# Performance work log

Hardware: AMD Instinct MI355X
Metric: run time of the kernel (lower is better)

## Reference

```python
import jax, jax.numpy as jnp
import numpy as np
from jax import lax

KERNEL = 2
STACKS = 2
LAYERS = 10
DILATIONS = [2 ** l for _ in range(STACKS) for l in range(LAYERS)]  # 20 blocks
RECEPTIVE_FIELD = sum((KERNEL - 1) * d for d in DILATIONS)  # 2046


def setup_inputs() -> dict:
    key = jax.random.key(0)
    ks = jax.random.split(key, 8)
    B, L, C, NC = 8, 4096, 256, 256
    NB = len(DILATIONS)
    SK = L - RECEPTIVE_FIELD  # 2050

    def rn(k, shape, scale):
        return jax.random.normal(k, shape, jnp.float32) * scale

    return {
        "input_x": jax.random.normal(ks[0], (B, L, 1), jnp.float32),
        "causal_w": rn(ks[1], (1, C), 1.0),                 # 1x1 causal conv, in=1
        "causal_b": jnp.zeros((C,), jnp.float32),
        "dil_w": rn(ks[2], (NB, KERNEL, C, C), (KERNEL * C) ** -0.5),  # WIO per block
        "dil_b": jnp.zeros((NB, C), jnp.float32),
        "res_w": rn(ks[3], (NB, C, C), C ** -0.5),
        "res_b": jnp.zeros((NB, C), jnp.float32),
        "skip_w": rn(ks[4], (NB, C, C), C ** -0.5),
        "skip_b": jnp.zeros((NB, C), jnp.float32),
        "cls_conv_w": rn(ks[5], (C, C), C ** -0.5),
        "cls_conv_b": jnp.zeros((C,), jnp.float32),
        "dense_w": rn(ks[6], (SK * C, NC), (SK * C) ** -0.5),
        "dense_b": jnp.zeros((NC,), jnp.float32),
    }


def _conv1x1(x, w, b):
    # x: [B, T, Cin], w: [Cin, Cout]
    return jnp.einsum("btc,co->bto", x, w) + b


def _dilated_causal_conv(x, w, b, d):
    # keras 'causal' pad followed by slicing off the first (k-1)*d frames
    # is exactly a VALID dilated conv. x: [B,T,Cin], w: [K,Cin,Cout]
    y = lax.conv_general_dilated(
        x, w, window_strides=(1,), padding="VALID", rhs_dilation=(d,),
        dimension_numbers=("NWC", "WIO", "NWC"))
    return y + b


def reference(input_x, causal_w, causal_b, dil_w, dil_b, res_w, res_b,
              skip_w, skip_b, cls_conv_w, cls_conv_b, dense_w, dense_b):
    # initial causal conv (kernel_size=1 -> plain 1x1 conv)
    x = _conv1x1(input_x, causal_w, causal_b)  # [B, L, C]
    skip_size = x.shape[1] - RECEPTIVE_FIELD

    skips = []
    for i, d in enumerate(DILATIONS):
        h = _dilated_causal_conv(x, dil_w[i], dil_b[i], d)  # [B, T-(k-1)d, C]
        g = jnp.tanh(h) * jax.nn.sigmoid(h)                  # gated activation
        res = _conv1x1(g, res_w[i], res_b[i])
        x = res + g                                          # residual (same length)
        s = _conv1x1(g, skip_w[i], skip_b[i])[:, -skip_size:]
        skips.append(s)

    # classifier head: mean over blocks, relu, shared 1x1 conv twice, dense+softmax
    s = jnp.mean(jnp.stack(skips, 0), axis=0)  # [B, skip_size, C]
    s = jax.nn.relu(s)
    s = _conv1x1(s, cls_conv_w, cls_conv_b)
    s = jax.nn.relu(s)
    s = _conv1x1(s, cls_conv_w, cls_conv_b)    # same conv applied twice (shared weights)
    f = s.reshape(s.shape[0], -1)              # flatten [B, skip_size*C]
    logits = f @ dense_w + dense_b
    return jax.nn.softmax(logits, axis=-1)
```

## Files before the change

### kernel.cpp

```cpp
#include <hip/hip_runtime.h>

typedef __attribute__((ext_vector_type(8))) short short8;
typedef __attribute__((ext_vector_type(4))) float f32x4;
typedef unsigned int uint32;
typedef unsigned short u16;

#define CCH   256
#define BATCH 8
#define LFULL 4096
#define SKL   2050
#define BM    64
#define BN    128
#define LDKC  72

#define GSTRIDE ((size_t)BATCH * LFULL * CCH)
#define XSTR    ((size_t)LFULL * CCH)
#define SSTR    ((size_t)SKL * CCH)
#define PSTR    ((size_t)BATCH * SKL * CCH)

__device__ const int TOUT[20] = {4095,4093,4089,4081,4065,4033,3969,3841,3585,3073,
                                 3072,3070,3066,3058,3042,3010,2946,2818,2562,2050};

__device__ __forceinline__ u16 f2b(float f) {
  uint32 u = __float_as_uint(f);
  u += 0x7fff + ((u >> 16) & 1);
  return (u16)(u >> 16);
}
__device__ __forceinline__ float gatef(float h) {
  float hc = fmaxf(h, -30.0f);
  float q = __expf(-hc);
  return (1.0f - q) * __builtin_amdgcn_rcpf(fmaf(q, q, 1.0f));
}
__device__ __forceinline__ void glds16(const void* g, void* l) {
  __builtin_amdgcn_global_load_lds(
      (const __attribute__((address_space(1))) void*)g,
      (__attribute__((address_space(3))) void*)l, 16, 0, 0);
}
__device__ __forceinline__ int xcd_swz(int orig, int nwg) {
  int xcd = orig & 7, idx = orig >> 3;
  int q = nwg >> 3, r = nwg & 7;
  int base = (xcd < r) ? xcd * (q + 1) : r * (q + 1) + (xcd - r) * q;
  return base + idx;
}

__global__ __launch_bounds__(256)
void prep_all(const float* __restrict__ res_w, const float* __restrict__ dil_w,
              const float* __restrict__ dil_b, const float* __restrict__ res_b,
              const float* __restrict__ causal_w, const float* __restrict__ causal_b,
              const float* __restrict__ skip_w, const float* __restrict__ cls_w,
              const float* __restrict__ skip_b,
              u16* __restrict__ DWP, float* __restrict__ Bc, float* __restrict__ U,
              u16* __restrict__ SWP, u16* __restrict__ CW, float* __restrict__ SBS) {
  __shared__ float As[32][256];
  const int bx = blockIdx.x;
  const int tid = threadIdx.x;

  if (bx < 304) {
    int chunk = bx & 7, tap = (bx >> 3) & 1, bi = bx >> 4;
    int i = bi + 1;
    int co = tid;
    int ci0 = chunk * 32;

    for (int idx = tid; idx < 32 * 256; idx += 256) {
      int r = idx >> 8, m = idx & 255;
      float v = res_w[((size_t)(bi * 256 + ci0 + r)) * 256 + m];
      if (ci0 + r == m) v += 1.0f;
      As[r][m] = v;
    }
    __syncthreads();

    float acc[32];
    #pragma unroll
    for (int r = 0; r < 32; ++r) acc[r] = 0.0f;

    const float* Wb = dil_w + ((size_t)(i * 2 + tap) * 256) * 256 + co;
    for (int m4 = 0; m4 < 64; ++m4) {
      const float* wp = Wb + (size_t)m4 * 4 * 256;
      float w0 = wp[0], w1 = wp[256], w2 = wp[512], w3 = wp[768];
      #pragma unroll
      for (int r = 0; r < 32; ++r) {
        float4 a = *(const float4*)&As[r][m4 * 4];
        acc[r] = fmaf(a.x, w0, acc[r]);
        acc[r] = fmaf(a.y, w1, acc[r]);
        acc[r] = fmaf(a.z, w2, acc[r]);
        acc[r] = fmaf(a.w, w3, acc[r]);
      }
    }
    int kb = tap * 8 + chunk;
    int kt = kb >> 1, ks = kb & 1;
    int ny = co >> 7, wn = (co >> 6) & 1, fn = (co >> 4) & 3, fr = co & 15;
    u16* ob = DWP + (size_t)bi * 131072 + kt * 16384 + ks * 8192 +
              ny * 4096 + wn * 2048 + fn * 512 + fr * 8;
    #pragma unroll
    for (int g = 0; g < 4; ++g) {
      u16 tmp[8];
      #pragma unroll
      for (int jj = 0; jj < 8; ++jj) tmp[jj] = f2b(acc[g * 8 + jj]);
      *(uint4*)(ob + g * 128) = *(uint4*)tmp;
    }
  } else if (bx < 304 + 5120) {
    int e = (bx - 304) * 256 + tid;
    int co = e & 255, ci = (e >> 8) & 255, i = e >> 16;
    int kk = ci >> 6, ks = (ci >> 5) & 1, fq = (ci >> 3) & 3, jj = ci & 7;
    int ny = co >> 7, wn = (co >> 6) & 1, fn = (co >> 4) & 3, fr = co & 15;
    int lane = fq * 16 + fr;
    SWP[(size_t)i * 65536 + kk * 16384 + ks * 8192 + ny * 4096 + wn * 2048 +
        fn * 512 + lane * 8 + jj] = f2b(skip_w[e]);
  } else if (bx < 304 + 5120 + 256) {
    int e = (bx - 5424) * 256 + tid;
    int co = e & 255, ci = e >> 8;
    CW[(size_t)co * 256 + ci] = f2b(cls_w[e]);
  } else if (bx < 5680 + 19) {
    int bi = bx - 5680, i = bi + 1, co = tid;
    float acc = dil_b[(size_t)i * 256 + co];
    const float* W0 = dil_w + ((size_t)(i * 2 + 0) * 256) * 256;
    const float* W1 = dil_w + ((size_t)(i * 2 + 1) * 256) * 256;
    for (int m = 0; m < 256; ++m) {
      float rb = res_b[(size_t)bi * 256 + m];
      acc = fmaf(rb, W0[(size_t)m * 256 + co] + W1[(size_t)m * 256 + co], acc);
    }
    Bc[(size_t)bi * 256 + co] = acc;
  } else if (bx == 5699) {
    int co = tid;
    float u0 = 0.f, u1 = 0.f, b0 = dil_b[co];
    for (int m = 0; m < 256; ++m) {
      float cwm = causal_w[m], cbm = causal_b[m];
      float w0 = dil_w[(size_t)m * 256 + co];
      float w1 = dil_w[(size_t)(256 + m) * 256 + co];
      u0 = fmaf(cwm, w0, u0);
      u1 = fmaf(cwm, w1, u1);
      b0 = fmaf(cbm, w0 + w1, b0);
    }
    U[co] = u0; U[256 + co] = u1; U[512 + co] = b0;
  } else {
    int n = tid;
    float s = 0.f;
    for (int i = 0; i < 20; ++i) s += skip_b[(size_t)i * 256 + n];
    SBS[n] = s;
  }
}

__global__ __launch_bounds__(256)
void g0_init(const float* __restrict__ in, const float* __restrict__ U,
             u16* __restrict__ G0) {
  int t = blockIdx.x, b = blockIdx.y, co = threadIdx.x;
  float x0 = in[(size_t)b * LFULL + t];
  float x1 = in[(size_t)b * LFULL + t + 1];
  float h = fmaf(x0, U[co], fmaf(x1, U[256 + co], U[512 + co]));
  G0[((size_t)b * LFULL + t) * CCH + co] = f2b(gatef(h));
}

__global__ __launch_bounds__(256)
void gatem(const u16* __restrict__ Ain, int d, int Tout, int ntile,
           const u16* __restrict__ Wp, const float* __restrict__ bias,
           u16* __restrict__ Gout) {
  __shared__ u16 As[3][BM * 64];

  const int tid = threadIdx.x;
  const int nwg = ntile * 16;
  const int wgid = xcd_swz(blockIdx.x, nwg);
  const int tx = wgid % ntile;
  const int rem = wgid / ntile;
  const int ny = rem & 1;
  const int bb = rem >> 1;

  const int t0 = tx * BM;
  const int n0 = ny * BN;
  const int lane = tid & 63, wv = tid >> 6;
  const int wm = wv >> 1, wn = wv & 1;
  const int fr = lane & 15, fq = lane >> 4;
  const int rl = lane >> 3;
  const int subx = ((lane & 7) ^ rl) * 8;
  const int rowb = wv * 16;

  const u16* Ab = Ain + (size_t)bb * XSTR;
  const u16* Wbase = Wp + (size_t)ny * 4096 + wn * 2048 + lane * 8;

  f32x4 acc[2][4];
  #pragma unroll
  for (int fn = 0; fn < 4; ++fn) {
    float4 bv = *(const float4*)&bias[n0 + wn * 64 + fn * 16 + fq * 4];
    #pragma unroll
    for (int fm = 0; fm < 2; ++fm) acc[fm][fn] = (f32x4){bv.x, bv.y, bv.z, bv.w};
  }

  auto STAGE_A = [&](int kt, int sel) {
    const int tap = kt >> 2, ks0 = (kt & 3) * 64;
    #pragma unroll
    for (int qq = 0; qq < 2; ++qq) {
      int rr = rowb + qq * 8 + rl;
      int t = t0 + rr;
      if (t > Tout - 1) t = Tout - 1;
      glds16(Ab + (size_t)(t + tap * d) * CCH + ks0 + subx,
             &As[sel][(rowb + qq * 8) * 64]);
    }
  };
  auto LOADB = [&](int kt, short8* br) {
    const u16* base = Wbase + (size_t)kt * 16384;
    #pragma unroll
    for (int ks = 0; ks < 2; ++ks)
      #pragma unroll
      for (int fn = 0; fn < 4; ++fn)
        br[fn * 2 + ks] = *(const short8*)(base + ks * 8192 + fn * 512);
  };

  short8 b0r[8], b1r[8];
  LOADB(0, b0r);
  STAGE_A(0, 0);
  STAGE_A(1, 1);

  #pragma unroll
  for (int kt = 0; kt < 8; ++kt) {
    short8* bc = (kt & 1) ? b1r : b0r;
    short8* bn = (kt & 1) ? b0r : b1r;
    if (kt < 7) LOADB(kt + 1, bn);
    if (kt < 6) {
      STAGE_A(kt + 2, (kt + 2) % 3);
      asm volatile("s_waitcnt vmcnt(12)" ::: "memory");
    } else if (kt == 6) {
      asm volatile("s_waitcnt vmcnt(10)" ::: "memory");
    } else {
      asm volatile("s_waitcnt vmcnt(0)" ::: "memory");
    }
    __builtin_amdgcn_s_barrier();
    __builtin_amdgcn_sched_barrier(0);

    const int cur = kt % 3;
    #pragma unroll
    for (int ks = 0; ks < 2; ++ks) {
      short8 af[2];
      #pragma unroll
      for (int fm = 0; fm < 2; ++fm) {
        int row = wm * 32 + fm * 16 + fr;
        af[fm] = *(const short8*)&As[cur][row * 64 + ((ks * 4 + fq) ^ (row & 7)) * 8];
      }
      #pragma unroll
      for (int fm = 0; fm < 2; ++fm)
        #pragma unroll
        for (int fn = 0; fn < 4; ++fn)
          acc[fm][fn] = __builtin_amdgcn_mfma_f32_16x16x32_bf16(
              bc[fn * 2 + ks], af[fm], acc[fm][fn], 0, 0, 0);
    }
    __builtin_amdgcn_s_barrier();
  }

  u16* Ob = Gout + (size_t)bb * XSTR;
  #pragma unroll
  for (int fm = 0; fm < 2; ++fm) {
    int t = t0 + wm * 32 + fm * 16 + fr;
    if (t >= Tout) continue;
    #pragma unroll
    for (int fn = 0; fn < 4; ++fn) {
      int c0 = n0 + wn * 64 + fn * 16 + fq * 4;
      f32x4 a = acc[fm][fn];
      uint32 p0 = (uint32)f2b(gatef(a[0])) | ((uint32)f2b(gatef(a[1])) << 16);
      uint32 p1 = (uint32)f2b(gatef(a[2])) | ((uint32)f2b(gatef(a[3])) << 16);
      uint2 pk; pk.x = p0; pk.y = p1;
      *(uint2*)(Ob + (size_t)t * CCH + c0) = pk;
    }
  }
}

__global__ __launch_bounds__(256)
void skipm(const u16* __restrict__ Gh, const u16* __restrict__ SWP,
           float* __restrict__ P) {
  __shared__ u16 As[3][BM * 64];

  const int tid = threadIdx.x;
  const int stile = 33;
  const int nwg = stile * 2 * 32;
  const int wgid = xcd_swz(blockIdx.x, nwg);
  const int tx = wgid % stile;
  const int rem = wgid / stile;
  const int ny = rem & 1;
  const int zz = rem >> 1;
  const int b = zz >> 2, j = zz & 3;

  const int t0 = tx * BM;
  const int n0 = ny * BN;
  const int lane = tid & 63, wv = tid >> 6;
  const int wm = wv >> 1, wn = wv & 1;
  const int fr = lane & 15, fq = lane >> 4;
  const int rl = lane >> 3;
  const int subx = ((lane & 7) ^ rl) * 8;
  const int rowb = wv * 16;

  const u16* Gb = Gh + (size_t)b * XSTR;
  const u16* Wbase = SWP + (size_t)ny * 4096 + wn * 2048 + lane * 8;

  f32x4 acc[2][4];
  #pragma unroll
  for (int fm = 0; fm < 2; ++fm)
    #pragma unroll
    for (int fn = 0; fn < 4; ++fn) acc[fm][fn] = (f32x4){0.f, 0.f, 0.f, 0.f};

  auto STAGE_A = [&](int kt, int sel) {
    const int i = j * 5 + (kt >> 2);
    const int toff = TOUT[i] - SKL;
    const int ks0 = (kt & 3) * 64;
    const u16* Gi = Gb + (size_t)i * GSTRIDE;
    #pragma unroll
    for (int qq = 0; qq < 2; ++qq) {
      int rr = rowb + qq * 8 + rl;
      int t = t0 + rr;
      if (t > SKL - 1) t = SKL - 1;
      glds16(Gi + (size_t)(toff + t) * CCH + ks0 + subx,
             &As[sel][(rowb + qq * 8) * 64]);
    }
  };
  auto LOADB = [&](int kt, short8* br) {
    const int i = j * 5 + (kt >> 2), kk = kt & 3;
    const u16* base = Wbase + (size_t)i * 65536 + kk * 16384;
    #pragma unroll
    for (int ks = 0; ks < 2; ++ks)
      #pragma unroll
      for (int fn = 0; fn < 4; ++fn)
        br[fn * 2 + ks] = *(const short8*)(base + ks * 8192 + fn * 512);
  };

  short8 b0r[8], b1r[8];
  LOADB(0, b0r);
  STAGE_A(0, 0);
  STAGE_A(1, 1);

  #pragma unroll
  for (int kt = 0; kt < 20; ++kt) {
    short8* bc = (kt & 1) ? b1r : b0r;
    short8* bn = (kt & 1) ? b0r : b1r;
    if (kt < 19) LOADB(kt + 1, bn);
    if (kt < 18) {
      STAGE_A(kt + 2, (kt + 2) % 3);
      asm volatile("s_waitcnt vmcnt(12)" ::: "memory");
    } else if (kt == 18) {
      asm volatile("s_waitcnt vmcnt(10)" ::: "memory");
    } else {
      asm volatile("s_waitcnt vmcnt(0)" ::: "memory");
    }
    __builtin_amdgcn_s_barrier();
    __builtin_amdgcn_sched_barrier(0);

    const int cur = kt % 3;
    #pragma unroll
    for (int ks = 0; ks < 2; ++ks) {
      short8 af[2];
      #pragma unroll
      for (int fm = 0; fm < 2; ++fm) {
        int row = wm * 32 + fm * 16 + fr;
        af[fm] = *(const short8*)&As[cur][row * 64 + ((ks * 4 + fq) ^ (row & 7)) * 8];
      }
      #pragma unroll
      for (int fm = 0; fm < 2; ++fm)
        #pragma unroll
        for (int fn = 0; fn < 4; ++fn)
          acc[fm][fn] = __builtin_amdgcn_mfma_f32_16x16x32_bf16(
              bc[fn * 2 + ks], af[fm], acc[fm][fn], 0, 0, 0);
    }
    __builtin_amdgcn_s_barrier();
  }

  float* Pj = P + (size_t)j * PSTR + (size_t)b * SSTR;
  #pragma unroll
  for (int fm = 0; fm < 2; ++fm) {
    int t = t0 + wm * 32 + fm * 16 + fr;
    if (t >= SKL) continue;
    #pragma unroll
    for (int fn = 0; fn < 4; ++fn) {
      int c0 = n0 + wn * 64 + fn * 16 + fq * 4;
      f32x4 a = acc[fm][fn];
      float4 o = {a[0], a[1], a[2], a[3]};
      *(float4*)(Pj + (size_t)t * CCH + c0) = o;
    }
  }
}

enum { MODE_CLS1 = 1, MODE_CLS2 = 2 };

template <int MODE>
__global__ __launch_bounds__(256)
void convm(const void* __restrict__ Ainv, long a_bstride,
           const u16* __restrict__ Wt, const float* __restrict__ bias,
           const float* __restrict__ extra,
           void* __restrict__ Out1, long out_bstride, int Tout) {
  __shared__ u16 As[128 * LDKC];
  __shared__ u16 Bs[128 * LDKC];

  const int tid = threadIdx.x;
  const int bb  = blockIdx.z;
  const int t0  = blockIdx.x * 128;
  const int n0  = blockIdx.y * 128;
  const int lane = tid & 63, wv = tid >> 6;
  const int wm = wv >> 1, wn = wv & 1;
  const int fr = lane & 15, fq = lane >> 4;

  f32x4 acc[4][4];
  #pragma unroll
  for (int fn = 0; fn < 4; ++fn) {
    float bv = bias[n0 + wn * 64 + fn * 16 + fr];
    #pragma unroll
    for (int fm = 0; fm < 4; ++fm) acc[fm][fn] = (f32x4){bv, bv, bv, bv};
  }

  for (int kt = 0; kt < 4; ++kt) {
    for (int idx = tid; idx < 1024; idx += 256) {
      int r = idx >> 3, c8 = idx & 7;
      int t = t0 + r; if (t > Tout - 1) t = Tout - 1;
      uint4 v;
      if constexpr (MODE == MODE_CLS1) {
        const float* p0 = (const float*)Ainv + (size_t)bb * a_bstride +
                          (size_t)t * CCH + kt * 64 + c8 * 8;
        float4 s0 = *(const float4*)p0;
        float4 s1 = *(const float4*)(p0 + 4);
        #pragma unroll
        for (int jj = 1; jj < 4; ++jj) {
          const float* pj = p0 + (size_t)jj * PSTR;
          float4 a0 = *(const float4*)pj;
          float4 a1 = *(const float4*)(pj + 4);
          s0.x += a0.x; s0.y += a0.y; s0.z += a0.z; s0.w += a0.w;
          s1.x += a1.x; s1.y += a1.y; s1.z += a1.z; s1.w += a1.w;
        }
        float4 e0 = *(const float4*)&extra[kt * 64 + c8 * 8];
        float4 e1 = *(const float4*)&extra[kt * 64 + c8 * 8 + 4];
        u16 tmp[8];
        tmp[0] = f2b(fmaxf((s0.x + e0.x) * 0.05f, 0.f));
        tmp[1] = f2b(fmaxf((s0.y + e0.y) * 0.05f, 0.f));
        tmp[2] = f2b(fmaxf((s0.z + e0.z) * 0.05f, 0.f));
        tmp[3] = f2b(fmaxf((s0.w + e0.w) * 0.05f, 0.f));
        tmp[4] = f2b(fmaxf((s1.x + e1.x) * 0.05f, 0.f));
        tmp[5] = f2b(fmaxf((s1.y + e1.y) * 0.05f, 0.f));
        tmp[6] = f2b(fmaxf((s1.z + e1.z) * 0.05f, 0.f));
        tmp[7] = f2b(fmaxf((s1.w + e1.w) * 0.05f, 0.f));
        v = *(uint4*)tmp;
      } else {
        const u16* sp = (const u16*)Ainv + (size_t)bb * a_bstride +
                        (size_t)t * CCH + kt * 64 + c8 * 8;
        uint4 raw = *(const uint4*)sp;
        u16 tmp[8];
        *(uint4*)tmp = raw;
        #pragma unroll
        for (int jj = 0; jj < 8; ++jj) tmp[jj] = (tmp[jj] & 0x8000) ? (u16)0 : tmp[jj];
        v = *(uint4*)tmp;
      }
      *(uint4*)&As[r * LDKC + c8 * 8] = v;
    }
    for (int idx = tid; idx < 1024; idx += 256) {
      int r = idx >> 3, c8 = idx & 7;
      const u16* sp = Wt + (size_t)(n0 + r) * 256 + kt * 64 + c8 * 8;
      *(uint4*)&Bs[r * LDKC + c8 * 8] = *(const uint4*)sp;
    }
    __syncthreads();

    #pragma unroll
    for (int ks = 0; ks < 2; ++ks) {
      short8 af[4], bfr[4];
      #pragma unroll
      for (int fm = 0; fm < 4; ++fm)
        af[fm] = *(const short8*)&As[(wm * 64 + fm * 16 + fr) * LDKC + ks * 32 + fq * 8];
      #pragma unroll
      for (int fn = 0; fn < 4; ++fn)
        bfr[fn] = *(const short8*)&Bs[(wn * 64 + fn * 16 + fr) * LDKC + ks * 32 + fq * 8];
      #pragma unroll
      for (int fm = 0; fm < 4; ++fm)
        #pragma unroll
        for (int fn = 0; fn < 4; ++fn)
          acc[fm][fn] = __builtin_amdgcn_mfma_f32_16x16x32_bf16(
              af[fm], bfr[fn], acc[fm][fn], 0, 0, 0);
    }
    __syncthreads();
  }

  #pragma unroll
  for (int fm = 0; fm < 4; ++fm) {
    int rbase = t0 + wm * 64 + fm * 16 + fq * 4;
    #pragma unroll
    for (int r = 0; r < 4; ++r) {
      int t = rbase + r;
      if (t >= Tout) continue;
      #pragma unroll
      for (int fn = 0; fn < 4; ++fn) {
        int c = n0 + wn * 64 + fn * 16 + fr;
        float a = acc[fm][fn][r];
        size_t oix = (size_t)bb * out_bstride + (size_t)t * CCH + c;
        if constexpr (MODE == MODE_CLS1) {
          ((u16*)Out1)[oix] = f2b(a);
        } else {
          ((float*)Out1)[oix] = a;
        }
      }
    }
  }
}

__global__ __launch_bounds__(256)
void dense_partial(const float* __restrict__ f, const float* __restrict__ W,
                   float* __restrict__ part) {
  int tstep = blockIdx.x;
  int n = threadIdx.x;
  __shared__ float fs[BATCH][CCH];
  for (int idx = threadIdx.x; idx < BATCH * CCH; idx += 256) {
    int b = idx >> 8, c = idx & 255;
    fs[b][c] = f[((size_t)b * SKL + tstep) * CCH + c];
  }
  __syncthreads();
  float acc[BATCH] = {0.f, 0.f, 0.f, 0.f, 0.f, 0.f, 0.f, 0.f};
  const float* Wr = W + (size_t)tstep * CCH * CCH;
  for (int ci = 0; ci < CCH; ++ci) {
    float w = Wr[(size_t)ci * CCH + n];
    #pragma unroll
    for (int b = 0; b < BATCH; ++b) acc[b] = fmaf(fs[b][ci], w, acc[b]);
  }
  #pragma unroll
  for (int b = 0; b < BATCH; ++b)
    part[((size_t)tstep * BATCH + b) * CCH + n] = acc[b];
}

__global__ __launch_bounds__(256)
void reduce_part(const float* __restrict__ part, float* __restrict__ part2) {
  int chunk = blockIdx.x, b = blockIdx.y, n = threadIdx.x;
  int c0 = chunk * 33;
  int c1 = c0 + 33; if (c1 > SKL) c1 = SKL;
  float s = 0.f;
  for (int c = c0; c < c1; ++c) s += part[((size_t)c * BATCH + b) * CCH + n];
  part2[((size_t)b * 64 + chunk) * CCH + n] = s;
}

__global__ __launch_bounds__(256)
void softmax_k(const float* __restrict__ part2, const float* __restrict__ db,
               float* __restrict__ out) {
  int b = blockIdx.x, n = threadIdx.x;
  float s = db[n];
  for (int ch = 0; ch < 64; ++ch) s += part2[((size_t)b * 64 + ch) * CCH + n];

  __shared__ float r4[4];
  __shared__ float mglob, sglob;
  int wid = n >> 6, lane = n & 63;

  float m = s;
  #pragma unroll
  for (int off = 1; off < 64; off <<= 1) m = fmaxf(m, __shfl_xor(m, off));
  if (lane == 0) r4[wid] = m;
  __syncthreads();
  if (n == 0) mglob = fmaxf(fmaxf(r4[0], r4[1]), fmaxf(r4[2], r4[3]));
  __syncthreads();

  float e = expf(s - mglob);
  float se = e;
  #pragma unroll
  for (int off = 1; off < 64; off <<= 1) se += __shfl_xor(se, off);
  if (lane == 0) r4[wid] = se;
  __syncthreads();
  if (n == 0) sglob = r4[0] + r4[1] + r4[2] + r4[3];
  __syncthreads();

  out[(size_t)b * CCH + n] = e / sglob;
}

extern "C" void kernel_launch(void* const* d_in, const int* in_sizes, int n_in,
                              void* d_out, int out_size, void* d_ws, size_t ws_size,
                              hipStream_t stream) {
  const float* input_x  = (const float*)d_in[0];
  const float* causal_w = (const float*)d_in[1];
  const float* causal_b = (const float*)d_in[2];
  const float* dil_w    = (const float*)d_in[3];
  const float* dil_b    = (const float*)d_in[4];
  const float* res_w    = (const float*)d_in[5];
  const float* res_b    = (const float*)d_in[6];
  const float* skip_w   = (const float*)d_in[7];
  const float* skip_b   = (const float*)d_in[8];
  const float* cls_w    = (const float*)d_in[9];
  const float* cls_b    = (const float*)d_in[10];
  const float* dense_w  = (const float*)d_in[11];
  const float* dense_b  = (const float*)d_in[12];
  float* out = (float*)d_out;

  char* p = (char*)d_ws;
  u16*   Gh    = (u16*)p;   p += GSTRIDE * 20 * 2;
  float* P     = (float*)p; p += PSTR * 4 * 4;
  u16*   S1    = (u16*)p;   p += (size_t)BATCH * SKL * CCH * 2;
  float* S2    = (float*)p; p += (size_t)BATCH * SKL * CCH * 4;
  float* PART  = (float*)p; p += (size_t)SKL * BATCH * CCH * 4;
  float* PART2 = (float*)p; p += (size_t)BATCH * 64 * CCH * 4;
  u16*   DWP   = (u16*)p;   p += (size_t)19 * 131072 * 2;
  float* Bc    = (float*)p; p += (size_t)19 * 256 * 4;
  u16*   SWP   = (u16*)p;   p += (size_t)20 * 65536 * 2;
  u16*   CW    = (u16*)p;   p += (size_t)256 * 256 * 2;
  float* U     = (float*)p; p += (size_t)768 * 4;
  float* SBS   = (float*)p; p += (size_t)256 * 4;

  static const int dil[20] = {1, 2, 4, 8, 16, 32, 64, 128, 256, 512,
                              1, 2, 4, 8, 16, 32, 64, 128, 256, 512};
  static const int tout_h[20] = {4095,4093,4089,4081,4065,4033,3969,3841,3585,3073,
                                 3072,3070,3066,3058,3042,3010,2946,2818,2562,2050};
  dim3 blk(256);

  prep_all<<<dim3(5701), blk, 0, stream>>>(
      res_w, dil_w, dil_b, res_b, causal_w, causal_b, skip_w, cls_w, skip_b,
      DWP, Bc, U, SWP, CW, SBS);

  g0_init<<<dim3(4095, BATCH), blk, 0, stream>>>(input_x, U, Gh);

  for (int i = 1; i < 20; ++i) {
    int Tout = tout_h[i];
    int ntile = (Tout + BM - 1) / BM;
    gatem<<<dim3(ntile * 16), blk, 0, stream>>>(
        Gh + (size_t)(i - 1) * GSTRIDE, dil[i], Tout, ntile,
        DWP + (size_t)(i - 1) * 131072, Bc + (size_t)(i - 1) * 256,
        Gh + (size_t)i * GSTRIDE);
  }

  skipm<<<dim3(33 * 2 * 32), blk, 0, stream>>>(Gh, SWP, P);

  const int ctile = (SKL + 127) / 128;
  convm<MODE_CLS1><<<dim3(ctile, 2, BATCH), blk, 0, stream>>>(
      P, (long)SSTR, CW, cls_b, SBS, S1, (long)SSTR, SKL);
  convm<MODE_CLS2><<<dim3(ctile, 2, BATCH), blk, 0, stream>>>(
      S1, (long)SSTR, CW, cls_b, nullptr, S2, (long)SSTR, SKL);

  dense_partial<<<dim3(SKL), blk, 0, stream>>>(S2, dense_w, PART);
  reduce_part<<<dim3(64, BATCH), blk, 0, stream>>>(PART, PART2);
  softmax_k<<<dim3(BATCH), blk, 0, stream>>>(PART2, dense_b, out);
}
```

Before: 670.9 us.

## Quad-buffer A tiles, fuse dense reduction, grid-stride g0 init

The GEMM kernels move to four LDS buffers for the A tile and drop the trailing barrier each k-step, since with four buffers the tile being staged no longer overwrites the one still being read. The dense layer now has each block accumulate 8 timesteps before writing partials, which removes the separate reduce kernel and the large partial buffer. g0_init becomes a grid-stride loop over 2048 blocks with the U values loaded once per thread. The aim is less barrier stall and fewer launches, at the cost of extra LDS use and a longer per-block dense loop.

```diff
diff --git a/kernel.cpp b/kernel.cpp
--- a/kernel.cpp
+++ b/kernel.cpp
@@ -12,6 +12,7 @@
 #define BM    64
 #define BN    128
 #define LDKC  72
+#define DCH   257
 
 #define GSTRIDE ((size_t)BATCH * LFULL * CCH)
 #define XSTR    ((size_t)LFULL * CCH)
@@ -143,18 +144,22 @@
 __global__ __launch_bounds__(256)
 void g0_init(const float* __restrict__ in, const float* __restrict__ U,
              u16* __restrict__ G0) {
-  int t = blockIdx.x, b = blockIdx.y, co = threadIdx.x;
-  float x0 = in[(size_t)b * LFULL + t];
-  float x1 = in[(size_t)b * LFULL + t + 1];
-  float h = fmaf(x0, U[co], fmaf(x1, U[256 + co], U[512 + co]));
-  G0[((size_t)b * LFULL + t) * CCH + co] = f2b(gatef(h));
+  int co = threadIdx.x;
+  float u0 = U[co], u1 = U[256 + co], b0 = U[512 + co];
+  for (int row = blockIdx.x; row < BATCH * 4095; row += 2048) {
+    int b = row / 4095, t = row - b * 4095;
+    float x0 = in[(size_t)b * LFULL + t];
+    float x1 = in[(size_t)b * LFULL + t + 1];
+    float h = fmaf(x0, u0, fmaf(x1, u1, b0));
+    G0[((size_t)b * LFULL + t) * CCH + co] = f2b(gatef(h));
+  }
 }
 
 __global__ __launch_bounds__(256)
 void gatem(const u16* __restrict__ Ain, int d, int Tout, int ntile,
            const u16* __restrict__ Wp, const float* __restrict__ bias,
            u16* __restrict__ Gout) {
-  __shared__ u16 As[3][BM * 64];
+  __shared__ u16 As[4][BM * 64];
 
   const int tid = threadIdx.x;
   const int nwg = ntile * 16;
@@ -215,7 +220,7 @@
     short8* bn = (kt & 1) ? b0r : b1r;
     if (kt < 7) LOADB(kt + 1, bn);
     if (kt < 6) {
-      STAGE_A(kt + 2, (kt + 2) % 3);
+      STAGE_A(kt + 2, (kt + 2) & 3);
       asm volatile("s_waitcnt vmcnt(12)" ::: "memory");
     } else if (kt == 6) {
       asm volatile("s_waitcnt vmcnt(10)" ::: "memory");
@@ -225,7 +230,7 @@
     __builtin_amdgcn_s_barrier();
     __builtin_amdgcn_sched_barrier(0);
 
-    const int cur = kt % 3;
+    const int cur = kt & 3;
     #pragma unroll
     for (int ks = 0; ks < 2; ++ks) {
       short8 af[2];
@@ -241,7 +246,6 @@
           acc[fm][fn] = __builtin_amdgcn_mfma_f32_16x16x32_bf16(
               bc[fn * 2 + ks], af[fm], acc[fm][fn], 0, 0, 0);
     }
-    __builtin_amdgcn_s_barrier();
   }
 
   u16* Ob = Gout + (size_t)bb * XSTR;
@@ -264,7 +268,7 @@
 __global__ __launch_bounds__(256)
 void skipm(const u16* __restrict__ Gh, const u16* __restrict__ SWP,
            float* __restrict__ P) {
-  __shared__ u16 As[3][BM * 64];
+  __shared__ u16 As[4][BM * 64];
 
   const int tid = threadIdx.x;
   const int stile = 33;
@@ -329,7 +333,7 @@
     short8* bn = (kt & 1) ? b0r : b1r;
     if (kt < 19) LOADB(kt + 1, bn);
     if (kt < 18) {
-      STAGE_A(kt + 2, (kt + 2) % 3);
+      STAGE_A(kt + 2, (kt + 2) & 3);
       asm volatile("s_waitcnt vmcnt(12)" ::: "memory");
     } else if (kt == 18) {
       asm volatile("s_waitcnt vmcnt(10)" ::: "memory");
@@ -339,7 +343,7 @@
     __builtin_amdgcn_s_barrier();
     __builtin_amdgcn_sched_barrier(0);
 
-    const int cur = kt % 3;
+    const int cur = kt & 3;
     #pragma unroll
     for (int ks = 0; ks < 2; ++ks) {
       short8 af[2];
@@ -355,7 +359,6 @@
           acc[fm][fn] = __builtin_amdgcn_mfma_f32_16x16x32_bf16(
               bc[fn * 2 + ks], af[fm], acc[fm][fn], 0, 0, 0);
     }
-    __builtin_amdgcn_s_barrier();
   }
 
   float* Pj = P + (size_t)j * PSTR + (size_t)b * SSTR;
@@ -491,36 +494,33 @@
 }
 
 __global__ __launch_bounds__(256)
-void dense_partial(const float* __restrict__ f, const float* __restrict__ W,
-                   float* __restrict__ part) {
-  int tstep = blockIdx.x;
+void dense2(const float* __restrict__ f, const float* __restrict__ W,
+            float* __restrict__ part2) {
+  int ch = blockIdx.x;
   int n = threadIdx.x;
+  int tcount = SKL - ch * 8; if (tcount > 8) tcount = 8;
   __shared__ float fs[BATCH][CCH];
-  for (int idx = threadIdx.x; idx < BATCH * CCH; idx += 256) {
-    int b = idx >> 8, c = idx & 255;
-    fs[b][c] = f[((size_t)b * SKL + tstep) * CCH + c];
-  }
-  __syncthreads();
   float acc[BATCH] = {0.f, 0.f, 0.f, 0.f, 0.f, 0.f, 0.f, 0.f};
-  const float* Wr = W + (size_t)tstep * CCH * CCH;
-  for (int ci = 0; ci < CCH; ++ci) {
-    float w = Wr[(size_t)ci * CCH + n];
-    #pragma unroll
-    for (int b = 0; b < BATCH; ++b) acc[b] = fmaf(fs[b][ci], w, acc[b]);
+
+  for (int tt = 0; tt < tcount; ++tt) {
+    int tstep = ch * 8 + tt;
+    __syncthreads();
+    for (int idx = n; idx < BATCH * CCH; idx += 256) {
+      int b = idx >> 8, c = idx & 255;
+      fs[b][c] = f[((size_t)b * SKL + tstep) * CCH + c];
+    }
+    __syncthreads();
+    const float* Wr = W + (size_t)tstep * CCH * CCH;
+    #pragma unroll 8
+    for (int ci = 0; ci < CCH; ++ci) {
+      float w = Wr[(size_t)ci * CCH + n];
+      #pragma unroll
+      for (int b = 0; b < BATCH; ++b) acc[b] = fmaf(fs[b][ci], w, acc[b]);
+    }
   }
   #pragma unroll
   for (int b = 0; b < BATCH; ++b)
-    part[((size_t)tstep * BATCH + b) * CCH + n] = acc[b];
-}
-
-__global__ __launch_bounds__(256)
-void reduce_part(const float* __restrict__ part, float* __restrict__ part2) {
-  int chunk = blockIdx.x, b = blockIdx.y, n = threadIdx.x;
-  int c0 = chunk * 33;
-  int c1 = c0 + 33; if (c1 > SKL) c1 = SKL;
-  float s = 0.f;
-  for (int c = c0; c < c1; ++c) s += part[((size_t)c * BATCH + b) * CCH + n];
-  part2[((size_t)b * 64 + chunk) * CCH + n] = s;
+    part2[((size_t)b * DCH + ch) * CCH + n] = acc[b];
 }
 
 __global__ __launch_bounds__(256)
@@ -528,7 +528,7 @@
                float* __restrict__ out) {
   int b = blockIdx.x, n = threadIdx.x;
   float s = db[n];
-  for (int ch = 0; ch < 64; ++ch) s += part2[((size_t)b * 64 + ch) * CCH + n];
+  for (int ch = 0; ch < DCH; ++ch) s += part2[((size_t)b * DCH + ch) * CCH + n];
 
   __shared__ float r4[4];
   __shared__ float mglob, sglob;
@@ -577,8 +577,7 @@
   float* P     = (float*)p; p += PSTR * 4 * 4;
   u16*   S1    = (u16*)p;   p += (size_t)BATCH * SKL * CCH * 2;
   float* S2    = (float*)p; p += (size_t)BATCH * SKL * CCH * 4;
-  float* PART  = (float*)p; p += (size_t)SKL * BATCH * CCH * 4;
-  float* PART2 = (float*)p; p += (size_t)BATCH * 64 * CCH * 4;
+  float* PART2 = (float*)p; p += (size_t)BATCH * DCH * CCH * 4;
   u16*   DWP   = (u16*)p;   p += (size_t)19 * 131072 * 2;
   float* Bc    = (float*)p; p += (size_t)19 * 256 * 4;
   u16*   SWP   = (u16*)p;   p += (size_t)20 * 65536 * 2;
@@ -596,7 +595,7 @@
       res_w, dil_w, dil_b, res_b, causal_w, causal_b, skip_w, cls_w, skip_b,
       DWP, Bc, U, SWP, CW, SBS);
 
-  g0_init<<<dim3(4095, BATCH), blk, 0, stream>>>(input_x, U, Gh);
+  g0_init<<<dim3(2048), blk, 0, stream>>>(input_x, U, Gh);
 
   for (int i = 1; i < 20; ++i) {
     int Tout = tout_h[i];
@@ -615,7 +614,6 @@
   convm<MODE_CLS2><<<dim3(ctile, 2, BATCH), blk, 0, stream>>>(
       S1, (long)SSTR, CW, cls_b, nullptr, S2, (long)SSTR, SKL);
 
-  dense_partial<<<dim3(SKL), blk, 0, stream>>>(S2, dense_w, PART);
-  reduce_part<<<dim3(64, BATCH), blk, 0, stream>>>(PART, PART2);
+  dense2<<<dim3(DCH), blk, 0, stream>>>(S2, dense_w, PART2);
   softmax_k<<<dim3(BATCH), blk, 0, stream>>>(PART2, dense_b, out);
 }
```

Result: slower. 732.1 us (+9.1%).
